# Kernel tuning notes

Measured on AMD Instinct MI355X. Metric: run time of the kernel, lower is better.

## Reference

```python
import jax, jax.numpy as jnp
import numpy as np

B = 8192      # batch of matchups
L = 40        # history_len
HN = 32       # hist_numeric_dim
TE = 96       # team_embed_dim
SE = 32       # seed_embed_dim
HH = 64       # hist_hidden_dim
NH = 4        # num_heads
HD = HH // NH # head dim = 16
MID = 128     # middle_dim
BOX = 8       # box_score_dim
NT = 400      # num_teams
NS = 17       # num_seeds
TOWER_IN = TE + SE + 1 + 2 * HH  # 257
MERGED = 2 * MID                 # 256
EPS = 1e-5


def setup_inputs() -> dict:
    key = jax.random.key(0)
    ks = iter(jax.random.split(key, 80))
    nrm = lambda shape, s=0.05: (jax.random.normal(next(ks), shape, jnp.float32) * s)
    inp = {}
    inp['teamA_id'] = jax.random.randint(next(ks), (B,), 1, NT)
    inp['teamB_id'] = jax.random.randint(next(ks), (B,), 1, NT)
    inp['teamA_seed'] = jax.random.randint(next(ks), (B,), 0, NS)
    inp['teamB_seed'] = jax.random.randint(next(ks), (B,), 0, NS)
    inp['teamA_elo'] = 1500.0 + 200.0 * jax.random.normal(next(ks), (B,), jnp.float32)
    inp['teamB_elo'] = 1500.0 + 200.0 * jax.random.normal(next(ks), (B,), jnp.float32)
    inp['teamA_hist_numeric'] = jax.random.normal(next(ks), (B, L, HN), jnp.float32)
    inp['teamB_hist_numeric'] = jax.random.normal(next(ks), (B, L, HN), jnp.float32)
    inp['teamA_hist_opp_ids'] = jax.random.randint(next(ks), (B, L), 0, NT)
    inp['teamB_hist_opp_ids'] = jax.random.randint(next(ks), (B, L), 0, NT)
    # 0/1 padding mask; guarantee at least one valid game per row
    inp['teamA_hist_mask'] = (jax.random.uniform(next(ks), (B, L)) < 0.8).astype(jnp.float32).at[:, 0].set(1.0)
    inp['teamB_hist_mask'] = (jax.random.uniform(next(ks), (B, L)) < 0.8).astype(jnp.float32).at[:, 0].set(1.0)
    # parameters
    inp['team_emb'] = nrm((NT, TE), 0.1).at[0].set(0.0)  # padding_idx=0
    inp['seed_emb'] = nrm((NS, SE), 0.1)
    inp['conv_w'] = nrm((HH, HN + TE, 3))
    inp['conv_b'] = nrm((HH,))
    inp['cbn_g'] = jnp.ones((HH,)); inp['cbn_b'] = jnp.zeros((HH,))
    inp['cbn_rm'] = nrm((HH,), 0.01); inp['cbn_rv'] = jnp.ones((HH,))
    inp['hp_w'] = nrm((HH, HN + TE)); inp['hp_b'] = nrm((HH,))
    inp['qp_w'] = nrm((HH, TE)); inp['qp_b'] = nrm((HH,))
    inp['attn_in_w'] = nrm((3 * HH, HH)); inp['attn_in_b'] = nrm((3 * HH,))
    inp['attn_out_w'] = nrm((HH, HH)); inp['attn_out_b'] = nrm((HH,))
    inp['ln_g'] = jnp.ones((HH,)); inp['ln_b'] = jnp.zeros((HH,))
    inp['tw_w'] = nrm((MID, TOWER_IN)); inp['tw_b'] = nrm((MID,))
    inp['tbn_g'] = jnp.ones((MID,)); inp['tbn_b'] = jnp.zeros((MID,))
    inp['tbn_rm'] = nrm((MID,), 0.01); inp['tbn_rv'] = jnp.ones((MID,))
    inp['r1_w'] = nrm((MERGED, MERGED)); inp['r1_b'] = nrm((MERGED,))
    inp['r1bn_g'] = jnp.ones((MERGED,)); inp['r1bn_b'] = jnp.zeros((MERGED,))
    inp['r1bn_rm'] = nrm((MERGED,), 0.01); inp['r1bn_rv'] = jnp.ones((MERGED,))
    inp['r2_w'] = nrm((MERGED, MERGED)); inp['r2_b'] = nrm((MERGED,))
    inp['r2bn_g'] = jnp.ones((MERGED,)); inp['r2bn_b'] = jnp.zeros((MERGED,))
    inp['r2bn_rm'] = nrm((MERGED,), 0.01); inp['r2bn_rv'] = jnp.ones((MERGED,))
    inp['mu_w'] = nrm((BOX, MERGED)); inp['mu_b'] = nrm((BOX,))
    inp['lv_w'] = nrm((BOX, MERGED)); inp['lv_b'] = nrm((BOX,))
    inp['wl_w'] = nrm((1, MERGED)); inp['wl_b'] = nrm((1,))
    return inp


def _bn(x, g, b, rm, rv):
    # eval-mode BatchNorm over last axis
    return (x - rm) * jax.lax.rsqrt(rv + EPS) * g + b


def _ln(x, g, b):
    m = jnp.mean(x, axis=-1, keepdims=True)
    v = jnp.var(x, axis=-1, keepdims=True)
    return (x - m) * jax.lax.rsqrt(v + EPS) * g + b


def reference(teamA_id, teamB_id, teamA_seed, teamB_seed, teamA_elo, teamB_elo,
              teamA_hist_numeric, teamA_hist_opp_ids, teamA_hist_mask,
              teamB_hist_numeric, teamB_hist_opp_ids, teamB_hist_mask,
              team_emb, seed_emb, conv_w, conv_b, cbn_g, cbn_b, cbn_rm, cbn_rv,
              hp_w, hp_b, qp_w, qp_b, attn_in_w, attn_in_b, attn_out_w, attn_out_b,
              ln_g, ln_b, tw_w, tw_b, tbn_g, tbn_b, tbn_rm, tbn_rv,
              r1_w, r1_b, r1bn_g, r1bn_b, r1bn_rm, r1bn_rv,
              r2_w, r2_b, r2bn_g, r2bn_b, r2bn_rm, r2bn_rv,
              mu_w, mu_b, lv_w, lv_b, wl_w, wl_b):
    silu = jax.nn.silu

    def attend(q_emb, hn, opp, mask):
        m = mask[..., None]
        x = jnp.concatenate([hn * m, team_emb[opp] * m], axis=-1)      # [B,L,HN+TE]
        res = silu(x @ hp_w.T + hp_b)                                   # [B,L,HH]
        c = jax.lax.conv_general_dilated(
            x.transpose(0, 2, 1), conv_w, (1,), [(1, 1)],
            dimension_numbers=('NCH', 'OIH', 'NCH')) + conv_b[:, None]  # [B,HH,L]
        c = _bn(c.transpose(0, 2, 1), cbn_g, cbn_b, cbn_rm, cbn_rv)     # [B,L,HH]
        kv = silu(c + res)                                              # [B,L,HH]
        q = q_emb @ qp_w.T + qp_b                                       # [B,HH]
        wq, wk, wv = jnp.split(attn_in_w, 3, axis=0)
        bq, bk, bv = jnp.split(attn_in_b, 3, axis=0)
        qh = (q @ wq.T + bq).reshape(-1, NH, HD)
        kh = (kv @ wk.T + bk).reshape(-1, L, NH, HD)
        vh = (kv @ wv.T + bv).reshape(-1, L, NH, HD)
        scores = jnp.einsum('bhd,blhd->bhl', qh, kh) / np.float32(np.sqrt(HD))
        scores = jnp.where(mask[:, None, :] > 0.0, scores, -1e9)
        a = jax.nn.softmax(scores, axis=-1)
        o = jnp.einsum('bhl,blhd->bhd', a, vh).reshape(-1, HH)
        o = o @ attn_out_w.T + attn_out_b
        return _ln(o + q, ln_g, ln_b)

    ea = team_emb[teamA_id]
    eb = team_emb[teamB_id]
    sa = seed_emb[teamA_seed]
    sb = seed_emb[teamB_seed]
    za = (teamA_elo[:, None] - 1500.0) / 400.0
    zb = (teamB_elo[:, None] - 1500.0) / 400.0

    aa = attend(ea, teamA_hist_numeric, teamA_hist_opp_ids, teamA_hist_mask)
    ab = attend(ea, teamB_hist_numeric, teamB_hist_opp_ids, teamB_hist_mask)
    bb = attend(eb, teamB_hist_numeric, teamB_hist_opp_ids, teamB_hist_mask)
    ba = attend(eb, teamA_hist_numeric, teamA_hist_opp_ids, teamA_hist_mask)

    ta = jnp.concatenate([ea, sa, za, aa, ab], axis=-1)
    tb = jnp.concatenate([eb, sb, zb, bb, ba], axis=-1)

    tower = lambda t: silu(_bn(t @ tw_w.T + tw_b, tbn_g, tbn_b, tbn_rm, tbn_rv))
    ra = tower(ta)
    rb = tower(tb)

    x = jnp.concatenate([ra - rb, ra * rb], axis=-1)
    x = silu(_bn(x @ r1_w.T + r1_b, r1bn_g, r1bn_b, r1bn_rm, r1bn_rv)) + x
    x = silu(_bn(x @ r2_w.T + r2_b, r2bn_g, r2bn_b, r2bn_rm, r2bn_rv)) + x

    box_mu = x @ mu_w.T + mu_b
    box_log_var = x @ lv_w.T + lv_b
    win_logit = (x @ wl_w.T + wl_b)[:, 0]
    return ((box_mu, box_log_var), win_logit)
```

## Files before the change

kernel.cpp:

```cpp
#include <hip/hip_runtime.h>
#include <stdint.h>

#define EPS 1e-5f

typedef __attribute__((ext_vector_type(8))) short short8;
typedef __attribute__((ext_vector_type(4))) float floatx4;
typedef __attribute__((ext_vector_type(4))) unsigned uintx4;
typedef unsigned short u16;

__device__ __forceinline__ u16 f2bf(float f) {
  unsigned u = __builtin_bit_cast(unsigned, f);
  u += 0x7fffu + ((u >> 16) & 1u);
  return (u16)(u >> 16);
}
__device__ __forceinline__ float bf2f(u16 h) {
  return __builtin_bit_cast(float, (unsigned)h << 16);
}
__device__ __forceinline__ unsigned pack2bf(float a, float b) {
  return (unsigned)f2bf(a) | ((unsigned)f2bf(b) << 16);
}
__device__ __forceinline__ float silu_f(float x) { return x / (1.f + __expf(-x)); }
__device__ __forceinline__ float wave_sum(float x) {
  for (int off = 32; off > 0; off >>= 1) x += __shfl_xor(x, off);
  return x;
}

__global__ void prep_kernel(const float* __restrict__ hp_w, const float* __restrict__ conv_w,
                            const float* __restrict__ attn_in_w,
                            const float* __restrict__ attn_out_w,
                            const float* __restrict__ tw_w, const float* __restrict__ r1_w,
                            const float* __restrict__ r2_w,
                            u16* __restrict__ w1f, u16* __restrict__ w2f,
                            float* __restrict__ woT,
                            float* __restrict__ twT, float* __restrict__ r1T,
                            float* __restrict__ r2T) {
  int t = blockIdx.x * 256 + threadIdx.x;
  if (t < 32768) {
    int j = t & 7, lane = (t >> 3) & 63, ks = (t >> 9) & 3, nt = (t >> 11) & 3, tp = t >> 13;
    int k = ks * 32 + ((lane >> 4) << 3) + j;
    int c = nt * 16 + (lane & 15);
    float v = (tp == 3) ? hp_w[c * 128 + k] : conv_w[c * 384 + k * 3 + tp];
    w1f[t] = f2bf(v);
  }
  if (t < 8192) {
    int j = t & 7, lane = (t >> 3) & 63, ks = (t >> 9) & 1, nt = t >> 10;
    int k = ks * 32 + ((lane >> 4) << 3) + j;
    int n = nt * 16 + (lane & 15);
    w2f[t] = f2bf(attn_in_w[(64 + n) * 64 + k]);
  }
  if (t < 1024) {
    int j = t & 63, k4 = t >> 6;
#pragma unroll
    for (int i = 0; i < 4; ++i)
      woT[(k4 * 64 + j) * 4 + i] = attn_out_w[j * 64 + k4 * 4 + i];
  }
  if (t < 8320) {
    int mid = t & 127, k4 = t >> 7;
#pragma unroll
    for (int i = 0; i < 4; ++i) {
      int k = k4 * 4 + i;
      twT[t * 4 + i] = (k < 257) ? tw_w[mid * 257 + k] : 0.f;
    }
  }
  if (t < 16384) {
    int o = t & 255, k4 = t >> 8;
#pragma unroll
    for (int i = 0; i < 4; ++i) {
      r1T[t * 4 + i] = r1_w[o * 256 + k4 * 4 + i];
      r2T[t * 4 + i] = r2_w[o * 256 + k4 * 4 + i];
    }
  }
}

__global__ __launch_bounds__(64) void team_kernel(
    const float* __restrict__ temb, const float* __restrict__ qp_w,
    const float* __restrict__ qp_b, const float* __restrict__ attn_in_w,
    const float* __restrict__ attn_in_b,
    float* __restrict__ Qg, float* __restrict__ QHg) {
  __shared__ float e[96];
  __shared__ float qv[64];
  const int t = blockIdx.x;
  const int o = threadIdx.x;
  for (int i = o; i < 96; i += 64) e[i] = temb[t * 96 + i];
  __syncthreads();
  float acc = qp_b[o];
  for (int k = 0; k < 96; ++k) acc += e[k] * qp_w[o * 96 + k];
  qv[o] = acc;
  Qg[t * 64 + o] = acc;
  __syncthreads();
  float acc2 = attn_in_b[o];
  for (int k = 0; k < 64; ++k) acc2 += qv[k] * attn_in_w[o * 64 + k];
  QHg[t * 64 + o] = acc2;
}

__global__ __launch_bounds__(256, 2) void attn_kernel(
    const int* __restrict__ idA, const int* __restrict__ idB,
    const float* __restrict__ hnA, const float* __restrict__ hnB,
    const int* __restrict__ oppA, const int* __restrict__ oppB,
    const float* __restrict__ mskA, const float* __restrict__ mskB,
    const float* __restrict__ temb, const float* __restrict__ conv_b,
    const float* __restrict__ cbn_g, const float* __restrict__ cbn_b,
    const float* __restrict__ cbn_rm, const float* __restrict__ cbn_rv,
    const float* __restrict__ hp_b,
    const float* __restrict__ attn_in_b, const float* __restrict__ attn_out_b,
    const float* __restrict__ ln_g, const float* __restrict__ ln_b,
    const u16* __restrict__ w1f, const u16* __restrict__ w2f,
    const float* __restrict__ woT,
    const float* __restrict__ Qg, const float* __restrict__ QHg,
    float* __restrict__ ATT) {
  __shared__ __align__(16) u16 arena[19488];
  u16* xs = arena;
  u16* kvb = arena + 5712;
  float* KVP = (float*)(arena + 9168);
  float* a_s = (float*)(arena + 5712);
  float* o_s = a_s + 8 * 40;
  float* qh_s = o_s + 2 * 64;

  const int tid = threadIdx.x;
  const int lane = tid & 63;
  const int wv = tid >> 6;
  const int qd = lane >> 4;
  const int l16 = lane & 15;

  const int c_lane = wv * 16 + l16;
  const float sc_c = rsqrtf(cbn_rv[c_lane] + EPS) * cbn_g[c_lane];
  const float sh_c = cbn_b[c_lane] - cbn_rm[c_lane] * sc_c;
  const float hpb_c = hp_b[c_lane];
  const float cvb_c = conv_b[c_lane];
  const float lng = ln_g[lane], lnb = ln_b[lane];
  const float aob = attn_out_b[lane];
  const float kb0 = attn_in_b[64 + (wv * 2 + 0) * 16 + l16];
  const float kb1 = attn_in_b[64 + (wv * 2 + 1) * 16 + l16];

  if (tid < 136) {
    xs[tid] = 0;
    xs[41 * 136 + tid] = 0;
  }
  __syncthreads();

  short8 w1r[4][4];
#pragma unroll
  for (int tp = 0; tp < 4; ++tp)
#pragma unroll
    for (int ks = 0; ks < 4; ++ks)
      w1r[tp][ks] = *reinterpret_cast<const short8*>(
          w1f + (((tp * 4 + wv) * 4 + ks) * 64 + lane) * 8);
  short8 w2r[2][2];
#pragma unroll
  for (int ntl = 0; ntl < 2; ++ntl)
#pragma unroll
    for (int ks = 0; ks < 2; ++ks)
      w2r[ntl][ks] = *reinterpret_cast<const short8*>(
          w2f + (((wv * 2 + ntl) * 2 + ks) * 64 + lane) * 8);

  unsigned xr[12];
  float mkr[3];
  {
    int np = blockIdx.x;
    int pb = np >> 1;
    const float* phn = (np & 1) ? hnB : hnA;
    const int* popp = (np & 1) ? oppB : oppA;
    const float* pmsk = (np & 1) ? mskB : mskA;
#pragma unroll
    for (int j = 0; j < 3; ++j) {
      int sidx = j * 256 + tid;
      int srow = sidx >> 4, scg = sidx & 15;
      if (srow < 40) {
        int mrow = pb * 40 + srow;
        mkr[j] = pmsk[mrow];
        const float* p = (scg < 4)
                             ? phn + (size_t)mrow * 32 + scg * 8
                             : temb + (size_t)popp[mrow] * 96 + (scg * 8 - 32);
        floatx4 f0 = *reinterpret_cast<const floatx4*>(p);
        floatx4 f1 = *reinterpret_cast<const floatx4*>(p + 4);
        xr[j * 4 + 0] = pack2bf(f0[0], f0[1]);
        xr[j * 4 + 1] = pack2bf(f0[2], f0[3]);
        xr[j * 4 + 2] = pack2bf(f1[0], f1[1]);
        xr[j * 4 + 3] = pack2bf(f1[2], f1[3]);
      } else {
        mkr[j] = 0.f;
        xr[j * 4 + 0] = xr[j * 4 + 1] = xr[j * 4 + 2] = xr[j * 4 + 3] = 0u;
      }
    }
  }

  float qreg = 0.f, qhreg = 0.f, m_l = 0.f;
  if (wv < 2) {
    int b0i = blockIdx.x >> 1, s0 = blockIdx.x & 1;
    int id0 = wv ? idB[b0i] : idA[b0i];
    qreg = Qg[id0 * 64 + lane];
    qhreg = QHg[id0 * 64 + lane];
    if (lane < 40) m_l = (s0 ? mskB : mskA)[b0i * 40 + lane];
  }

#pragma unroll 1
  for (int it = 0; it < 8; ++it) {
    int pair = blockIdx.x + it * 2048;
    int b = pair >> 1, s = pair & 1;

#pragma unroll
    for (int j = 0; j < 3; ++j) {
      int sidx = j * 256 + tid;
      int srow = sidx >> 4;
      if (srow < 40) {
        bool keep = mkr[j] != 0.f;
        uintx4 v;
        v[0] = keep ? xr[j * 4 + 0] : 0u;
        v[1] = keep ? xr[j * 4 + 1] : 0u;
        v[2] = keep ? xr[j * 4 + 2] : 0u;
        v[3] = keep ? xr[j * 4 + 3] : 0u;
        *reinterpret_cast<uintx4*>(xs + (srow + 1) * 136 + (sidx & 15) * 8) = v;
      }
    }
    __syncthreads();

    float pf[3][8];
    float mknew[3];
    {
      int np = (it < 7) ? pair + 2048 : pair;
      int pb = np >> 1;
      const float* phn = (np & 1) ? hnB : hnA;
      const int* popp = (np & 1) ? oppB : oppA;
      const float* pmsk = (np & 1) ? mskB : mskA;
#pragma unroll
      for (int j = 0; j < 3; ++j) {
        int sidx = j * 256 + tid;
        int srow = sidx >> 4, scg = sidx & 15;
        if (srow < 40) {
          int mrow = pb * 40 + srow;
          mknew[j] = pmsk[mrow];
          const float* p = (scg < 4)
                               ? phn + (size_t)mrow * 32 + scg * 8
                               : temb + (size_t)popp[mrow] * 96 + (scg * 8 - 32);
          *reinterpret_cast<floatx4*>(&pf[j][0]) = *reinterpret_cast<const floatx4*>(p);
          *reinterpret_cast<floatx4*>(&pf[j][4]) = *reinterpret_cast<const floatx4*>(p + 4);
        } else {
          mknew[j] = 0.f;
#pragma unroll
          for (int q = 0; q < 8; ++q) pf[j][q] = 0.f;
        }
      }
    }

#pragma unroll 1
    for (int mt = 0; mt < 3; ++mt) {
      floatx4 ach = {0.f, 0.f, 0.f, 0.f};
      floatx4 acv = {0.f, 0.f, 0.f, 0.f};
#pragma unroll
      for (int ks = 0; ks < 4; ++ks) {
        const u16* base = xs + (mt * 16 + l16) * 136 + ks * 32 + (qd << 3);
        short8 af0 = *reinterpret_cast<const short8*>(base);
        short8 af1 = *reinterpret_cast<const short8*>(base + 136);
        short8 af2 = *reinterpret_cast<const short8*>(base + 272);
        acv = __builtin_amdgcn_mfma_f32_16x16x32_bf16(af0, w1r[0][ks], acv, 0, 0, 0);
        acv = __builtin_amdgcn_mfma_f32_16x16x32_bf16(af1, w1r[1][ks], acv, 0, 0, 0);
        acv = __builtin_amdgcn_mfma_f32_16x16x32_bf16(af2, w1r[2][ks], acv, 0, 0, 0);
        ach = __builtin_amdgcn_mfma_f32_16x16x32_bf16(af1, w1r[3][ks], ach, 0, 0, 0);
      }
#pragma unroll
      for (int r = 0; r < 4; ++r) {
        float kv = silu_f(silu_f(ach[r] + hpb_c) + (acv[r] + cvb_c) * sc_c + sh_c);
        kvb[(mt * 16 + qd * 4 + r) * 72 + c_lane] = f2bf(kv);
      }
    }
    __syncthreads();

    {
      floatx4 acc[3][2] = {};
#pragma unroll
      for (int mt = 0; mt < 3; ++mt) {
        short8 af[2];
#pragma unroll
        for (int ks = 0; ks < 2; ++ks)
          af[ks] = *reinterpret_cast<const short8*>(
              kvb + (mt * 16 + l16) * 72 + ks * 32 + (qd << 3));
#pragma unroll
        for (int ntl = 0; ntl < 2; ++ntl)
#pragma unroll
          for (int ks = 0; ks < 2; ++ks)
            acc[mt][ntl] = __builtin_amdgcn_mfma_f32_16x16x32_bf16(
                af[ks], w2r[ntl][ks], acc[mt][ntl], 0, 0, 0);
      }
#pragma unroll
      for (int mt = 0; mt < 3; ++mt)
#pragma unroll
        for (int ntl = 0; ntl < 2; ++ntl)
#pragma unroll
          for (int r = 0; r < 4; ++r) {
            int row = mt * 16 + qd * 4 + r;
            if (row < 40)
              KVP[row * 129 + (wv * 2 + ntl) * 16 + l16] =
                  acc[mt][ntl][r] + (ntl ? kb1 : kb0);
          }
    }
    __syncthreads();

#pragma unroll
    for (int j = 0; j < 3; ++j) {
      xr[j * 4 + 0] = pack2bf(pf[j][0], pf[j][1]);
      xr[j * 4 + 1] = pack2bf(pf[j][2], pf[j][3]);
      xr[j * 4 + 2] = pack2bf(pf[j][4], pf[j][5]);
      xr[j * 4 + 3] = pack2bf(pf[j][6], pf[j][7]);
      mkr[j] = mknew[j];
    }

    if (wv < 2) {
      int qi = wv;
      qh_s[qi * 64 + lane] = qhreg;
      float a[4];
#pragma unroll
      for (int h = 0; h < 4; ++h) {
        float e = 0.f;
        if (lane < 40 && m_l > 0.f) {
          float s0 = 0.f, s1 = 0.f;
#pragma unroll
          for (int d = 0; d < 16; d += 2) {
            s0 += qh_s[qi * 64 + h * 16 + d] * KVP[lane * 129 + h * 16 + d];
            s1 += qh_s[qi * 64 + h * 16 + d + 1] * KVP[lane * 129 + h * 16 + d + 1];
          }
          e = __expf((s0 + s1) * 0.25f);
        }
        float sm = wave_sum(e);
        a[h] = e / sm;
      }
#pragma unroll
      for (int h = 0; h < 4; ++h)
        if (lane < 40) a_s[(qi * 4 + h) * 40 + lane] = a[h];
      {
        int p = qi * 4 + (lane >> 4);
        float v0 = 0.f, v1 = 0.f;
#pragma unroll
        for (int l = 0; l < 40; l += 2) {
          v0 += a_s[p * 40 + l] * KVP[l * 129 + 64 + lane];
          v1 += a_s[p * 40 + l + 1] * KVP[(l + 1) * 129 + 64 + lane];
        }
        o_s[qi * 64 + lane] = v0 + v1;
      }
      float acc0 = aob + qreg, acc1 = 0.f;
      const floatx4* wo4 = reinterpret_cast<const floatx4*>(woT);
#pragma unroll 8
      for (int k4 = 0; k4 < 16; ++k4) {
        floatx4 w4 = wo4[k4 * 64 + lane];
        floatx4 x4 = *reinterpret_cast<const floatx4*>(&o_s[qi * 64 + k4 * 4]);
        acc0 += x4[0] * w4[0] + x4[2] * w4[2];
        acc1 += x4[1] * w4[1] + x4[3] * w4[3];
      }
      float r = acc0 + acc1;
      float mean = wave_sum(r) * (1.f / 64.f);
      float dv = r - mean;
      float var = wave_sum(dv * dv) * (1.f / 64.f);
      float outv = dv * rsqrtf(var + EPS) * lng + lnb;
      ATT[((qi * 2 + s) * 8192 + b) * 64 + lane] = outv;

      if (it < 7) {
        int bn = b + 1024;
        int idn = wv ? idB[bn] : idA[bn];
        qreg = Qg[idn * 64 + lane];
        qhreg = QHg[idn * 64 + lane];
        m_l = (lane < 40) ? (s ? mskB : mskA)[bn * 40 + lane] : 0.f;
      }
    }
  }
}

__global__ __launch_bounds__(256) void head_kernel(
    const int* __restrict__ idA, const int* __restrict__ idB,
    const int* __restrict__ seedA, const int* __restrict__ seedB,
    const float* __restrict__ eloA, const float* __restrict__ eloB,
    const float* __restrict__ temb, const float* __restrict__ semb,
    const float* __restrict__ twT, const float* __restrict__ tw_b,
    const float* __restrict__ tbn_g, const float* __restrict__ tbn_b,
    const float* __restrict__ tbn_rm, const float* __restrict__ tbn_rv,
    const float* __restrict__ r1T, const float* __restrict__ r1_b,
    const float* __restrict__ r1bn_g, const float* __restrict__ r1bn_b,
    const float* __restrict__ r1bn_rm, const float* __restrict__ r1bn_rv,
    const float* __restrict__ r2T, const float* __restrict__ r2_b,
    const float* __restrict__ r2bn_g, const float* __restrict__ r2bn_b,
    const float* __restrict__ r2bn_rm, const float* __restrict__ r2bn_rv,
    const float* __restrict__ mu_w, const float* __restrict__ mu_b,
    const float* __restrict__ lv_w, const float* __restrict__ lv_b,
    const float* __restrict__ wl_w, const float* __restrict__ wl_b,
    const float* __restrict__ ATT, float* __restrict__ out) {
  __shared__ __align__(16) float smem[12416];
  float* tv = smem;
  float* rr = smem + 8320;
  float* xv = smem;
  float* xw = smem + 4096;
  const int tid = threadIdx.x;
  const int b0 = blockIdx.x * 16;

  for (int idx = tid; idx < 2 * 16 * 260; idx += 256) {
    int k = idx % 260;
    int bi = (idx / 260) & 15;
    int team = idx / (260 * 16);
    int b = b0 + bi;
    float v;
    if (k < 96) v = temb[(team ? idB[b] : idA[b]) * 96 + k];
    else if (k < 128) v = semb[(team ? seedB[b] : seedA[b]) * 32 + (k - 96)];
    else if (k == 128) v = ((team ? eloB[b] : eloA[b]) - 1500.f) * (1.f / 400.f);
    else if (k < 193) v = ATT[((team * 2 + team) * 8192 + b) * 64 + (k - 129)];
    else if (k < 257) v = ATT[((team * 2 + (1 - team)) * 8192 + b) * 64 + (k - 193)];
    else v = 0.f;
    tv[(team * 16 + bi) * 260 + k] = v;
  }
  __syncthreads();

  {
    int team = tid >> 7, mid = tid & 127;
    const floatx4* twv = reinterpret_cast<const floatx4*>(twT);
    float acc[16];
    float b_ = tw_b[mid];
#pragma unroll
    for (int bi = 0; bi < 16; ++bi) acc[bi] = b_;
#pragma unroll 2
    for (int k4 = 0; k4 < 65; ++k4) {
      floatx4 w4 = twv[k4 * 128 + mid];
#pragma unroll
      for (int bi = 0; bi < 16; ++bi) {
        floatx4 x4 = *reinterpret_cast<const floatx4*>(&tv[(team * 16 + bi) * 260 + k4 * 4]);
        acc[bi] += x4[0] * w4[0] + x4[1] * w4[1] + x4[2] * w4[2] + x4[3] * w4[3];
      }
    }
    float sc = rsqrtf(tbn_rv[mid] + EPS) * tbn_g[mid];
    float sh = tbn_b[mid] - tbn_rm[mid] * sc;
#pragma unroll
    for (int bi = 0; bi < 16; ++bi)
      rr[(team * 16 + bi) * 128 + mid] = silu_f(acc[bi] * sc + sh);
  }
  __syncthreads();
  {
    int o = tid;
#pragma unroll
    for (int bi = 0; bi < 16; ++bi)
      xv[bi * 256 + o] = (o < 128)
                             ? (rr[bi * 128 + o] - rr[(16 + bi) * 128 + o])
                             : (rr[bi * 128 + o - 128] * rr[(16 + bi) * 128 + o - 128]);
  }
  __syncthreads();
  {
    int o = tid;
    const floatx4* r1v = reinterpret_cast<const floatx4*>(r1T);
    float acc[16];
    float b_ = r1_b[o];
#pragma unroll
    for (int bi = 0; bi < 16; ++bi) acc[bi] = b_;
#pragma unroll 2
    for (int k4 = 0; k4 < 64; ++k4) {
      floatx4 w4 = r1v[k4 * 256 + o];
#pragma unroll
      for (int bi = 0; bi < 16; ++bi) {
        floatx4 x4 = *reinterpret_cast<const floatx4*>(&xv[bi * 256 + k4 * 4]);
        acc[bi] += x4[0] * w4[0] + x4[1] * w4[1] + x4[2] * w4[2] + x4[3] * w4[3];
      }
    }
    float sc = rsqrtf(r1bn_rv[o] + EPS) * r1bn_g[o];
    float sh = r1bn_b[o] - r1bn_rm[o] * sc;
#pragma unroll
    for (int bi = 0; bi < 16; ++bi)
      xw[bi * 256 + o] = silu_f(acc[bi] * sc + sh) + xv[bi * 256 + o];
  }
  __syncthreads();
  {
    int o = tid;
    const floatx4* r2v = reinterpret_cast<const floatx4*>(r2T);
    float acc[16];
    float b_ = r2_b[o];
#pragma unroll
    for (int bi = 0; bi < 16; ++bi) acc[bi] = b_;
#pragma unroll 2
    for (int k4 = 0; k4 < 64; ++k4) {
      floatx4 w4 = r2v[k4 * 256 + o];
#pragma unroll
      for (int bi = 0; bi < 16; ++bi) {
        floatx4 x4 = *reinterpret_cast<const floatx4*>(&xw[bi * 256 + k4 * 4]);
        acc[bi] += x4[0] * w4[0] + x4[1] * w4[1] + x4[2] * w4[2] + x4[3] * w4[3];
      }
    }
    float sc = rsqrtf(r2bn_rv[o] + EPS) * r2bn_g[o];
    float sh = r2bn_b[o] - r2bn_rm[o] * sc;
#pragma unroll
    for (int bi = 0; bi < 16; ++bi)
      xv[bi * 256 + o] = silu_f(acc[bi] * sc + sh) + xw[bi * 256 + o];
  }
  __syncthreads();
  {
    int bi = tid >> 4, j = tid & 15;
    const float* wrow = (j < 8) ? (mu_w + j * 256) : (lv_w + (j - 8) * 256);
    const floatx4* wrow4 = reinterpret_cast<const floatx4*>(wrow);
    float acc = (j < 8) ? mu_b[j] : lv_b[j - 8];
#pragma unroll 4
    for (int k4 = 0; k4 < 64; ++k4) {
      floatx4 x4 = *reinterpret_cast<const floatx4*>(&xv[bi * 256 + k4 * 4]);
      floatx4 w4 = wrow4[k4];
      acc += x4[0] * w4[0] + x4[1] * w4[1] + x4[2] * w4[2] + x4[3] * w4[3];
    }
    int b = b0 + bi;
    if (j < 8) out[b * 8 + j] = acc;
    else out[65536 + b * 8 + (j - 8)] = acc;
    if (tid < 16) {
      const floatx4* wl4 = reinterpret_cast<const floatx4*>(wl_w);
      float acc2 = wl_b[0];
#pragma unroll 4
      for (int k4 = 0; k4 < 64; ++k4) {
        floatx4 x4 = *reinterpret_cast<const floatx4*>(&xv[tid * 256 + k4 * 4]);
        floatx4 w4 = wl4[k4];
        acc2 += x4[0] * w4[0] + x4[1] * w4[1] + x4[2] * w4[2] + x4[3] * w4[3];
      }
      out[131072 + b0 + tid] = acc2;
    }
  }
}

extern "C" void kernel_launch(void* const* d_in, const int* in_sizes, int n_in,
                              void* d_out, int out_size, void* d_ws, size_t ws_size,
                              hipStream_t stream) {
  const int* idA = (const int*)d_in[0];
  const int* idB = (const int*)d_in[1];
  const int* seedA = (const int*)d_in[2];
  const int* seedB = (const int*)d_in[3];
  const float* eloA = (const float*)d_in[4];
  const float* eloB = (const float*)d_in[5];
  const float* hnA = (const float*)d_in[6];
  const float* hnB = (const float*)d_in[7];
  const int* oppA = (const int*)d_in[8];
  const int* oppB = (const int*)d_in[9];
  const float* mskA = (const float*)d_in[10];
  const float* mskB = (const float*)d_in[11];
  const float* temb = (const float*)d_in[12];
  const float* semb = (const float*)d_in[13];
  const float* conv_w = (const float*)d_in[14];
  const float* conv_b = (const float*)d_in[15];
  const float* cbn_g = (const float*)d_in[16];
  const float* cbn_b = (const float*)d_in[17];
  const float* cbn_rm = (const float*)d_in[18];
  const float* cbn_rv = (const float*)d_in[19];
  const float* hp_w = (const float*)d_in[20];
  const float* hp_b = (const float*)d_in[21];
  const float* qp_w = (const float*)d_in[22];
  const float* qp_b = (const float*)d_in[23];
  const float* attn_in_w = (const float*)d_in[24];
  const float* attn_in_b = (const float*)d_in[25];
  const float* attn_out_w = (const float*)d_in[26];
  const float* attn_out_b = (const float*)d_in[27];
  const float* ln_g = (const float*)d_in[28];
  const float* ln_b = (const float*)d_in[29];
  const float* tw_w = (const float*)d_in[30];
  const float* tw_b = (const float*)d_in[31];
  const float* tbn_g = (const float*)d_in[32];
  const float* tbn_b = (const float*)d_in[33];
  const float* tbn_rm = (const float*)d_in[34];
  const float* tbn_rv = (const float*)d_in[35];
  const float* r1_w = (const float*)d_in[36];
  const float* r1_b = (const float*)d_in[37];
  const float* r1bn_g = (const float*)d_in[38];
  const float* r1bn_b = (const float*)d_in[39];
  const float* r1bn_rm = (const float*)d_in[40];
  const float* r1bn_rv = (const float*)d_in[41];
  const float* r2_w = (const float*)d_in[42];
  const float* r2_b = (const float*)d_in[43];
  const float* r2bn_g = (const float*)d_in[44];
  const float* r2bn_b = (const float*)d_in[45];
  const float* r2bn_rm = (const float*)d_in[46];
  const float* r2bn_rv = (const float*)d_in[47];
  const float* mu_w = (const float*)d_in[48];
  const float* mu_b = (const float*)d_in[49];
  const float* lv_w = (const float*)d_in[50];
  const float* lv_b = (const float*)d_in[51];
  const float* wl_w = (const float*)d_in[52];
  const float* wl_b = (const float*)d_in[53];

  char* ws = (char*)d_ws;
  u16* w1f = (u16*)(ws + 0);
  u16* w2f = (u16*)(ws + 65536);
  float* woT = (float*)(ws + 81920);
  float* Qg = (float*)(ws + 98304);
  float* QHg = (float*)(ws + 200704);
  float* twT = (float*)(ws + 303104);
  float* r1T = (float*)(ws + 436224);
  float* r2T = (float*)(ws + 698368);
  float* ATT = (float*)(ws + 960512);

  prep_kernel<<<256, 256, 0, stream>>>(hp_w, conv_w, attn_in_w, attn_out_w,
                                       tw_w, r1_w, r2_w,
                                       w1f, w2f, woT, twT, r1T, r2T);
  team_kernel<<<400, 64, 0, stream>>>(temb, qp_w, qp_b, attn_in_w, attn_in_b, Qg, QHg);
  attn_kernel<<<2048, 256, 0, stream>>>(idA, idB, hnA, hnB, oppA, oppB, mskA, mskB,
                                        temb, conv_b, cbn_g, cbn_b, cbn_rm, cbn_rv,
                                        hp_b, attn_in_b, attn_out_b, ln_g, ln_b,
                                        w1f, w2f, woT, Qg, QHg, ATT);
  head_kernel<<<512, 256, 0, stream>>>(idA, idB, seedA, seedB, eloA, eloB, temb, semb,
                                       twT, tw_b, tbn_g, tbn_b, tbn_rm, tbn_rv,
                                       r1T, r1_b, r1bn_g, r1bn_b, r1bn_rm, r1bn_rv,
                                       r2T, r2_b, r2bn_g, r2bn_b, r2bn_rm, r2bn_rv,
                                       mu_w, mu_b, lv_w, lv_b, wl_w, wl_b,
                                       ATT, (float*)d_out);
}
```

Baseline: 558.4 us.

## Spread attention epilogue across all four waves instead of two

The per-row attention tail (scores, softmax, weighted sum of values, output projection) previously ran on only two of four waves while the others idled. Now each wave handles two heads of one query, half of the value positions, and half of the output-projection K range. Partial results are combined through shared memory, and the layer norm stays on two waves. This adds three block-wide barriers per iteration and extra LDS traffic in exchange for better wave utilisation.

```diff
diff --git a/kernel.cpp b/kernel.cpp
--- a/kernel.cpp
+++ b/kernel.cpp
@@ -109,18 +109,21 @@
     const float* __restrict__ Qg, const float* __restrict__ QHg,
     float* __restrict__ ATT) {
   __shared__ __align__(16) u16 arena[19488];
+  __shared__ __align__(16) float qh_s[2 * 64];
   u16* xs = arena;
   u16* kvb = arena + 5712;
   float* KVP = (float*)(arena + 9168);
   float* a_s = (float*)(arena + 5712);
-  float* o_s = a_s + 8 * 40;
-  float* qh_s = o_s + 2 * 64;
+  float* op = a_s + 8 * 40;
+  float* rp = op + 2 * 2 * 64;
 
   const int tid = threadIdx.x;
   const int lane = tid & 63;
   const int wv = tid >> 6;
   const int qd = lane >> 4;
   const int l16 = lane & 15;
+  const int qw = wv >> 1;
+  const int hw = wv & 1;
 
   const int c_lane = wv * 16 + l16;
   const float sc_c = rsqrtf(cbn_rv[c_lane] + EPS) * cbn_g[c_lane];
@@ -185,12 +188,14 @@
   }
 
   float qreg = 0.f, qhreg = 0.f, m_l = 0.f;
-  if (wv < 2) {
+  {
     int b0i = blockIdx.x >> 1, s0 = blockIdx.x & 1;
-    int id0 = wv ? idB[b0i] : idA[b0i];
-    qreg = Qg[id0 * 64 + lane];
-    qhreg = QHg[id0 * 64 + lane];
     if (lane < 40) m_l = (s0 ? mskB : mskA)[b0i * 40 + lane];
+    if (wv < 2) {
+      int id0 = wv ? idB[b0i] : idA[b0i];
+      qreg = Qg[id0 * 64 + lane];
+      qhreg = QHg[id0 * 64 + lane];
+    }
   }
 
 #pragma unroll 1
@@ -198,6 +203,7 @@
     int pair = blockIdx.x + it * 2048;
     int b = pair >> 1, s = pair & 1;
 
+    if (wv < 2) qh_s[wv * 64 + lane] = qhreg;
 #pragma unroll
     for (int j = 0; j < 3; ++j) {
       int sidx = j * 256 + tid;
@@ -304,60 +310,77 @@
       mkr[j] = mknew[j];
     }
 
-    if (wv < 2) {
-      int qi = wv;
-      qh_s[qi * 64 + lane] = qhreg;
-      float a[4];
-#pragma unroll
-      for (int h = 0; h < 4; ++h) {
+    {
+      float a2[2];
+#pragma unroll
+      for (int hh = 0; hh < 2; ++hh) {
+        int h = hw * 2 + hh;
         float e = 0.f;
         if (lane < 40 && m_l > 0.f) {
           float s0 = 0.f, s1 = 0.f;
 #pragma unroll
           for (int d = 0; d < 16; d += 2) {
-            s0 += qh_s[qi * 64 + h * 16 + d] * KVP[lane * 129 + h * 16 + d];
-            s1 += qh_s[qi * 64 + h * 16 + d + 1] * KVP[lane * 129 + h * 16 + d + 1];
+            s0 += qh_s[qw * 64 + h * 16 + d] * KVP[lane * 129 + h * 16 + d];
+            s1 += qh_s[qw * 64 + h * 16 + d + 1] * KVP[lane * 129 + h * 16 + d + 1];
           }
           e = __expf((s0 + s1) * 0.25f);
         }
         float sm = wave_sum(e);
-        a[h] = e / sm;
-      }
-#pragma unroll
-      for (int h = 0; h < 4; ++h)
-        if (lane < 40) a_s[(qi * 4 + h) * 40 + lane] = a[h];
-      {
-        int p = qi * 4 + (lane >> 4);
-        float v0 = 0.f, v1 = 0.f;
-#pragma unroll
-        for (int l = 0; l < 40; l += 2) {
-          v0 += a_s[p * 40 + l] * KVP[l * 129 + 64 + lane];
-          v1 += a_s[p * 40 + l + 1] * KVP[(l + 1) * 129 + 64 + lane];
-        }
-        o_s[qi * 64 + lane] = v0 + v1;
-      }
-      float acc0 = aob + qreg, acc1 = 0.f;
+        a2[hh] = e / sm;
+      }
+      if (lane < 40) {
+        a_s[(qw * 4 + hw * 2 + 0) * 40 + lane] = a2[0];
+        a_s[(qw * 4 + hw * 2 + 1) * 40 + lane] = a2[1];
+      }
+    }
+    __syncthreads();
+
+    {
+      int p = qw * 4 + (lane >> 4);
+      int l0 = hw * 20;
+      float v0 = 0.f, v1 = 0.f;
+#pragma unroll
+      for (int l = l0; l < l0 + 20; l += 2) {
+        v0 += a_s[p * 40 + l] * KVP[l * 129 + 64 + lane];
+        v1 += a_s[p * 40 + l + 1] * KVP[(l + 1) * 129 + 64 + lane];
+      }
+      op[(qw * 2 + hw) * 64 + lane] = v0 + v1;
+    }
+    __syncthreads();
+
+    {
+      float acc0 = 0.f, acc1 = 0.f;
       const floatx4* wo4 = reinterpret_cast<const floatx4*>(woT);
-#pragma unroll 8
-      for (int k4 = 0; k4 < 16; ++k4) {
+#pragma unroll
+      for (int k4 = hw * 8; k4 < hw * 8 + 8; ++k4) {
         floatx4 w4 = wo4[k4 * 64 + lane];
-        floatx4 x4 = *reinterpret_cast<const floatx4*>(&o_s[qi * 64 + k4 * 4]);
-        acc0 += x4[0] * w4[0] + x4[2] * w4[2];
-        acc1 += x4[1] * w4[1] + x4[3] * w4[3];
-      }
-      float r = acc0 + acc1;
+        floatx4 xa = *reinterpret_cast<const floatx4*>(&op[(qw * 2 + 0) * 64 + k4 * 4]);
+        floatx4 xb = *reinterpret_cast<const floatx4*>(&op[(qw * 2 + 1) * 64 + k4 * 4]);
+        acc0 += (xa[0] + xb[0]) * w4[0] + (xa[2] + xb[2]) * w4[2];
+        acc1 += (xa[1] + xb[1]) * w4[1] + (xa[3] + xb[3]) * w4[3];
+      }
+      rp[(qw * 2 + hw) * 64 + lane] = acc0 + acc1;
+    }
+    __syncthreads();
+
+    if (wv < 2) {
+      int qi = wv;
+      float r = rp[(qi * 2 + 0) * 64 + lane] + rp[(qi * 2 + 1) * 64 + lane] +
+                aob + qreg;
       float mean = wave_sum(r) * (1.f / 64.f);
       float dv = r - mean;
       float var = wave_sum(dv * dv) * (1.f / 64.f);
       float outv = dv * rsqrtf(var + EPS) * lng + lnb;
       ATT[((qi * 2 + s) * 8192 + b) * 64 + lane] = outv;
-
-      if (it < 7) {
-        int bn = b + 1024;
+    }
+
+    if (it < 7) {
+      int bn = b + 1024;
+      if (lane < 40) m_l = (s ? mskB : mskA)[bn * 40 + lane];
+      if (wv < 2) {
         int idn = wv ? idB[bn] : idA[bn];
         qreg = Qg[idn * 64 + lane];
         qhreg = QHg[idn * 64 + lane];
-        m_l = (lane < 40) ? (s ? mskB : mskA)[bn * 40 + lane] : 0.f;
       }
     }
   }
```

Result: faster. 531.1 us (-4.9%).

## Process two histories per iteration so all four waves run attention

Applied to the files above, without the earlier changes.

The attention kernel now handles two batch rows per loop iteration, with double-buffered shared staging and KV buffers, so all four waves run the softmax/output stage (one query per wave) instead of only two waves working while the others idle. Iterations halve from 8 to 4, prefetch covers two rows plus the next query data, and __syncthreads is replaced with an explicit lgkmcnt wait plus s_barrier. Shared memory roughly doubles and register pressure rises from the doubled prefetch arrays, which may reduce occupancy under the 2-blocks-per-CU launch bound.

```diff
diff --git a/kernel.cpp b/kernel.cpp
--- a/kernel.cpp
+++ b/kernel.cpp
@@ -24,6 +24,12 @@
   for (int off = 32; off > 0; off >>= 1) x += __shfl_xor(x, off);
   return x;
 }
+
+#define BARRIER()                                         \
+  do {                                                    \
+    asm volatile("s_waitcnt lgkmcnt(0)" ::: "memory");    \
+    __builtin_amdgcn_s_barrier();                         \
+  } while (0)
 
 __global__ void prep_kernel(const float* __restrict__ hp_w, const float* __restrict__ conv_w,
                             const float* __restrict__ attn_in_w,
@@ -108,19 +114,30 @@
     const float* __restrict__ woT,
     const float* __restrict__ Qg, const float* __restrict__ QHg,
     float* __restrict__ ATT) {
-  __shared__ __align__(16) u16 arena[19488];
-  u16* xs = arena;
-  u16* kvb = arena + 5712;
-  float* KVP = (float*)(arena + 9168);
-  float* a_s = (float*)(arena + 5712);
-  float* o_s = a_s + 8 * 40;
-  float* qh_s = o_s + 2 * 64;
+  __shared__ __align__(16) u16 arena[38976];
+  __shared__ __align__(16) float qh_s[4 * 64];
+  u16* xs0 = arena;
+  u16* xs1 = arena + 5712;
+  u16* kvb0 = arena + 11424;
+  u16* kvb1 = arena + 14880;
+  float* KVP = (float*)(arena + 18336);
+  float* a_s = (float*)(arena + 11424);
+  float* op = a_s + 640;
 
   const int tid = threadIdx.x;
   const int lane = tid & 63;
   const int wv = tid >> 6;
   const int qd = lane >> 4;
   const int l16 = lane & 15;
+  const int tw = wv >> 1;
+  const int qi = wv & 1;
+
+  const int s = blockIdx.x & 1;
+  const int bbase = blockIdx.x >> 1;
+  const float* phn = s ? hnB : hnA;
+  const int* popp = s ? oppB : oppA;
+  const float* pmsk = s ? mskB : mskA;
+  const int* pid = qi ? idB : idA;
 
   const int c_lane = wv * 16 + l16;
   const float sc_c = rsqrtf(cbn_rv[c_lane] + EPS) * cbn_g[c_lane];
@@ -133,10 +150,11 @@
   const float kb1 = attn_in_b[64 + (wv * 2 + 1) * 16 + l16];
 
   if (tid < 136) {
-    xs[tid] = 0;
-    xs[41 * 136 + tid] = 0;
-  }
-  __syncthreads();
+    xs0[tid] = 0;
+    xs0[41 * 136 + tid] = 0;
+    xs1[tid] = 0;
+    xs1[41 * 136 + tid] = 0;
+  }
 
   short8 w1r[4][4];
 #pragma unroll
@@ -153,119 +171,136 @@
       w2r[ntl][ks] = *reinterpret_cast<const short8*>(
           w2f + (((wv * 2 + ntl) * 2 + ks) * 64 + lane) * 8);
 
-  unsigned xr[12];
-  float mkr[3];
-  {
-    int np = blockIdx.x;
-    int pb = np >> 1;
-    const float* phn = (np & 1) ? hnB : hnA;
-    const int* popp = (np & 1) ? oppB : oppA;
-    const float* pmsk = (np & 1) ? mskB : mskA;
+  unsigned xr[2][12];
+  float mkr[2][3];
+#pragma unroll
+  for (int t = 0; t < 2; ++t) {
+    int pb = bbase + t * 1024;
 #pragma unroll
     for (int j = 0; j < 3; ++j) {
       int sidx = j * 256 + tid;
       int srow = sidx >> 4, scg = sidx & 15;
       if (srow < 40) {
         int mrow = pb * 40 + srow;
-        mkr[j] = pmsk[mrow];
+        mkr[t][j] = pmsk[mrow];
         const float* p = (scg < 4)
                              ? phn + (size_t)mrow * 32 + scg * 8
                              : temb + (size_t)popp[mrow] * 96 + (scg * 8 - 32);
         floatx4 f0 = *reinterpret_cast<const floatx4*>(p);
         floatx4 f1 = *reinterpret_cast<const floatx4*>(p + 4);
-        xr[j * 4 + 0] = pack2bf(f0[0], f0[1]);
-        xr[j * 4 + 1] = pack2bf(f0[2], f0[3]);
-        xr[j * 4 + 2] = pack2bf(f1[0], f1[1]);
-        xr[j * 4 + 3] = pack2bf(f1[2], f1[3]);
+        xr[t][j * 4 + 0] = pack2bf(f0[0], f0[1]);
+        xr[t][j * 4 + 1] = pack2bf(f0[2], f0[3]);
+        xr[t][j * 4 + 2] = pack2bf(f1[0], f1[1]);
+        xr[t][j * 4 + 3] = pack2bf(f1[2], f1[3]);
       } else {
-        mkr[j] = 0.f;
-        xr[j * 4 + 0] = xr[j * 4 + 1] = xr[j * 4 + 2] = xr[j * 4 + 3] = 0u;
-      }
-    }
-  }
-
-  float qreg = 0.f, qhreg = 0.f, m_l = 0.f;
-  if (wv < 2) {
-    int b0i = blockIdx.x >> 1, s0 = blockIdx.x & 1;
-    int id0 = wv ? idB[b0i] : idA[b0i];
+        mkr[t][j] = 0.f;
+        xr[t][j * 4 + 0] = xr[t][j * 4 + 1] = xr[t][j * 4 + 2] = xr[t][j * 4 + 3] = 0u;
+      }
+    }
+  }
+
+  float qreg, qhreg, m_l = 0.f;
+  {
+    int b0 = bbase + tw * 1024;
+    int id0 = pid[b0];
     qreg = Qg[id0 * 64 + lane];
     qhreg = QHg[id0 * 64 + lane];
-    if (lane < 40) m_l = (s0 ? mskB : mskA)[b0i * 40 + lane];
-  }
+    if (lane < 40) m_l = pmsk[b0 * 40 + lane];
+  }
+  BARRIER();
 
 #pragma unroll 1
-  for (int it = 0; it < 8; ++it) {
-    int pair = blockIdx.x + it * 2048;
-    int b = pair >> 1, s = pair & 1;
-
-#pragma unroll
-    for (int j = 0; j < 3; ++j) {
-      int sidx = j * 256 + tid;
-      int srow = sidx >> 4;
-      if (srow < 40) {
-        bool keep = mkr[j] != 0.f;
-        uintx4 v;
-        v[0] = keep ? xr[j * 4 + 0] : 0u;
-        v[1] = keep ? xr[j * 4 + 1] : 0u;
-        v[2] = keep ? xr[j * 4 + 2] : 0u;
-        v[3] = keep ? xr[j * 4 + 3] : 0u;
-        *reinterpret_cast<uintx4*>(xs + (srow + 1) * 136 + (sidx & 15) * 8) = v;
-      }
-    }
-    __syncthreads();
-
-    float pf[3][8];
-    float mknew[3];
-    {
-      int np = (it < 7) ? pair + 2048 : pair;
-      int pb = np >> 1;
-      const float* phn = (np & 1) ? hnB : hnA;
-      const int* popp = (np & 1) ? oppB : oppA;
-      const float* pmsk = (np & 1) ? mskB : mskA;
+  for (int it = 0; it < 4; ++it) {
+    int bt0 = bbase + (2 * it) * 1024;
+    int bt1 = bt0 + 1024;
+    int b_w = bbase + (2 * it + tw) * 1024;
+
+#pragma unroll
+    for (int t = 0; t < 2; ++t) {
+      u16* xsd = t ? xs1 : xs0;
 #pragma unroll
       for (int j = 0; j < 3; ++j) {
         int sidx = j * 256 + tid;
-        int srow = sidx >> 4, scg = sidx & 15;
+        int srow = sidx >> 4;
         if (srow < 40) {
-          int mrow = pb * 40 + srow;
-          mknew[j] = pmsk[mrow];
-          const float* p = (scg < 4)
-                               ? phn + (size_t)mrow * 32 + scg * 8
-                               : temb + (size_t)popp[mrow] * 96 + (scg * 8 - 32);
-          *reinterpret_cast<floatx4*>(&pf[j][0]) = *reinterpret_cast<const floatx4*>(p);
-          *reinterpret_cast<floatx4*>(&pf[j][4]) = *reinterpret_cast<const floatx4*>(p + 4);
-        } else {
-          mknew[j] = 0.f;
-#pragma unroll
-          for (int q = 0; q < 8; ++q) pf[j][q] = 0.f;
+          bool keep = mkr[t][j] != 0.f;
+          uintx4 v;
+          v[0] = keep ? xr[t][j * 4 + 0] : 0u;
+          v[1] = keep ? xr[t][j * 4 + 1] : 0u;
+          v[2] = keep ? xr[t][j * 4 + 2] : 0u;
+          v[3] = keep ? xr[t][j * 4 + 3] : 0u;
+          *reinterpret_cast<uintx4*>(xsd + (srow + 1) * 136 + (sidx & 15) * 8) = v;
         }
       }
     }
+    BARRIER();
+
+    float pf[2][3][8];
+    float mknew[2][3];
+    float qn, qhn, m_n = 0.f;
+    {
+      int adv = (it < 3) ? 2048 : 0;
+#pragma unroll
+      for (int t = 0; t < 2; ++t) {
+        int pb = (t ? bt1 : bt0) + adv;
+#pragma unroll
+        for (int j = 0; j < 3; ++j) {
+          int sidx = j * 256 + tid;
+          int srow = sidx >> 4, scg = sidx & 15;
+          if (srow < 40) {
+            int mrow = pb * 40 + srow;
+            mknew[t][j] = pmsk[mrow];
+            const float* p = (scg < 4)
+                                 ? phn + (size_t)mrow * 32 + scg * 8
+                                 : temb + (size_t)popp[mrow] * 96 + (scg * 8 - 32);
+            *reinterpret_cast<floatx4*>(&pf[t][j][0]) = *reinterpret_cast<const floatx4*>(p);
+            *reinterpret_cast<floatx4*>(&pf[t][j][4]) = *reinterpret_cast<const floatx4*>(p + 4);
+          } else {
+            mknew[t][j] = 0.f;
+#pragma unroll
+            for (int q = 0; q < 8; ++q) pf[t][j][q] = 0.f;
+          }
+        }
+      }
+      int bn = b_w + adv;
+      int idn = pid[bn];
+      qn = Qg[idn * 64 + lane];
+      qhn = QHg[idn * 64 + lane];
+      if (lane < 40) m_n = pmsk[bn * 40 + lane];
+    }
 
 #pragma unroll 1
-    for (int mt = 0; mt < 3; ++mt) {
-      floatx4 ach = {0.f, 0.f, 0.f, 0.f};
-      floatx4 acv = {0.f, 0.f, 0.f, 0.f};
-#pragma unroll
-      for (int ks = 0; ks < 4; ++ks) {
-        const u16* base = xs + (mt * 16 + l16) * 136 + ks * 32 + (qd << 3);
-        short8 af0 = *reinterpret_cast<const short8*>(base);
-        short8 af1 = *reinterpret_cast<const short8*>(base + 136);
-        short8 af2 = *reinterpret_cast<const short8*>(base + 272);
-        acv = __builtin_amdgcn_mfma_f32_16x16x32_bf16(af0, w1r[0][ks], acv, 0, 0, 0);
-        acv = __builtin_amdgcn_mfma_f32_16x16x32_bf16(af1, w1r[1][ks], acv, 0, 0, 0);
-        acv = __builtin_amdgcn_mfma_f32_16x16x32_bf16(af2, w1r[2][ks], acv, 0, 0, 0);
-        ach = __builtin_amdgcn_mfma_f32_16x16x32_bf16(af1, w1r[3][ks], ach, 0, 0, 0);
-      }
-#pragma unroll
-      for (int r = 0; r < 4; ++r) {
-        float kv = silu_f(silu_f(ach[r] + hpb_c) + (acv[r] + cvb_c) * sc_c + sh_c);
-        kvb[(mt * 16 + qd * 4 + r) * 72 + c_lane] = f2bf(kv);
-      }
-    }
-    __syncthreads();
-
-    {
+    for (int t = 0; t < 2; ++t) {
+      const u16* xsrc = t ? xs1 : xs0;
+      u16* kdst = t ? kvb1 : kvb0;
+#pragma unroll 1
+      for (int mt = 0; mt < 3; ++mt) {
+        floatx4 ach = {0.f, 0.f, 0.f, 0.f};
+        floatx4 acv = {0.f, 0.f, 0.f, 0.f};
+#pragma unroll
+        for (int ks = 0; ks < 4; ++ks) {
+          const u16* base = xsrc + (mt * 16 + l16) * 136 + ks * 32 + (qd << 3);
+          short8 af0 = *reinterpret_cast<const short8*>(base);
+          short8 af1 = *reinterpret_cast<const short8*>(base + 136);
+          short8 af2 = *reinterpret_cast<const short8*>(base + 272);
+          acv = __builtin_amdgcn_mfma_f32_16x16x32_bf16(af0, w1r[0][ks], acv, 0, 0, 0);
+          acv = __builtin_amdgcn_mfma_f32_16x16x32_bf16(af1, w1r[1][ks], acv, 0, 0, 0);
+          acv = __builtin_amdgcn_mfma_f32_16x16x32_bf16(af2, w1r[2][ks], acv, 0, 0, 0);
+          ach = __builtin_amdgcn_mfma_f32_16x16x32_bf16(af1, w1r[3][ks], ach, 0, 0, 0);
+        }
+#pragma unroll
+        for (int r = 0; r < 4; ++r) {
+          float kv = silu_f(silu_f(ach[r] + hpb_c) + (acv[r] + cvb_c) * sc_c + sh_c);
+          kdst[(mt * 16 + qd * 4 + r) * 72 + c_lane] = f2bf(kv);
+        }
+      }
+    }
+    BARRIER();
+
+#pragma unroll 1
+    for (int t = 0; t < 2; ++t) {
+      const u16* ksrc = t ? kvb1 : kvb0;
+      float* Kp = KVP + t * 40 * 129;
       floatx4 acc[3][2] = {};
 #pragma unroll
       for (int mt = 0; mt < 3; ++mt) {
@@ -273,7 +308,7 @@
 #pragma unroll
         for (int ks = 0; ks < 2; ++ks)
           af[ks] = *reinterpret_cast<const short8*>(
-              kvb + (mt * 16 + l16) * 72 + ks * 32 + (qd << 3));
+              ksrc + (mt * 16 + l16) * 72 + ks * 32 + (qd << 3));
 #pragma unroll
         for (int ntl = 0; ntl < 2; ++ntl)
 #pragma unroll
@@ -289,25 +324,16 @@
           for (int r = 0; r < 4; ++r) {
             int row = mt * 16 + qd * 4 + r;
             if (row < 40)
-              KVP[row * 129 + (wv * 2 + ntl) * 16 + l16] =
+              Kp[row * 129 + (wv * 2 + ntl) * 16 + l16] =
                   acc[mt][ntl][r] + (ntl ? kb1 : kb0);
           }
     }
-    __syncthreads();
-
-#pragma unroll
-    for (int j = 0; j < 3; ++j) {
-      xr[j * 4 + 0] = pack2bf(pf[j][0], pf[j][1]);
-      xr[j * 4 + 1] = pack2bf(pf[j][2], pf[j][3]);
-      xr[j * 4 + 2] = pack2bf(pf[j][4], pf[j][5]);
-      xr[j * 4 + 3] = pack2bf(pf[j][6], pf[j][7]);
-      mkr[j] = mknew[j];
-    }
-
-    if (wv < 2) {
-      int qi = wv;
-      qh_s[qi * 64 + lane] = qhreg;
-      float a[4];
+    BARRIER();
+
+    {
+      const float* Kp = KVP + tw * 40 * 129;
+      qh_s[wv * 64 + lane] = qhreg;
+      float a4[4];
 #pragma unroll
       for (int h = 0; h < 4; ++h) {
         float e = 0.f;
@@ -315,33 +341,33 @@
           float s0 = 0.f, s1 = 0.f;
 #pragma unroll
           for (int d = 0; d < 16; d += 2) {
-            s0 += qh_s[qi * 64 + h * 16 + d] * KVP[lane * 129 + h * 16 + d];
-            s1 += qh_s[qi * 64 + h * 16 + d + 1] * KVP[lane * 129 + h * 16 + d + 1];
+            s0 += qh_s[wv * 64 + h * 16 + d] * Kp[lane * 129 + h * 16 + d];
+            s1 += qh_s[wv * 64 + h * 16 + d + 1] * Kp[lane * 129 + h * 16 + d + 1];
           }
           e = __expf((s0 + s1) * 0.25f);
         }
         float sm = wave_sum(e);
-        a[h] = e / sm;
+        a4[h] = e / sm;
       }
 #pragma unroll
       for (int h = 0; h < 4; ++h)
-        if (lane < 40) a_s[(qi * 4 + h) * 40 + lane] = a[h];
+        if (lane < 40) a_s[(wv * 4 + h) * 40 + lane] = a4[h];
       {
-        int p = qi * 4 + (lane >> 4);
+        int arow = wv * 4 + (lane >> 4);
         float v0 = 0.f, v1 = 0.f;
 #pragma unroll
         for (int l = 0; l < 40; l += 2) {
-          v0 += a_s[p * 40 + l] * KVP[l * 129 + 64 + lane];
-          v1 += a_s[p * 40 + l + 1] * KVP[(l + 1) * 129 + 64 + lane];
+          v0 += a_s[arow * 40 + l] * Kp[l * 129 + 64 + lane];
+          v1 += a_s[arow * 40 + l + 1] * Kp[(l + 1) * 129 + 64 + lane];
         }
-        o_s[qi * 64 + lane] = v0 + v1;
+        op[wv * 64 + lane] = v0 + v1;
       }
       float acc0 = aob + qreg, acc1 = 0.f;
       const floatx4* wo4 = reinterpret_cast<const floatx4*>(woT);
 #pragma unroll 8
       for (int k4 = 0; k4 < 16; ++k4) {
         floatx4 w4 = wo4[k4 * 64 + lane];
-        floatx4 x4 = *reinterpret_cast<const floatx4*>(&o_s[qi * 64 + k4 * 4]);
+        floatx4 x4 = *reinterpret_cast<const floatx4*>(&op[wv * 64 + k4 * 4]);
         acc0 += x4[0] * w4[0] + x4[2] * w4[2];
         acc1 += x4[1] * w4[1] + x4[3] * w4[3];
       }
@@ -350,16 +376,22 @@
       float dv = r - mean;
       float var = wave_sum(dv * dv) * (1.f / 64.f);
       float outv = dv * rsqrtf(var + EPS) * lng + lnb;
-      ATT[((qi * 2 + s) * 8192 + b) * 64 + lane] = outv;
-
-      if (it < 7) {
-        int bn = b + 1024;
-        int idn = wv ? idB[bn] : idA[bn];
-        qreg = Qg[idn * 64 + lane];
-        qhreg = QHg[idn * 64 + lane];
-        m_l = (lane < 40) ? (s ? mskB : mskA)[bn * 40 + lane] : 0.f;
-      }
-    }
+      ATT[((qi * 2 + s) * 8192 + b_w) * 64 + lane] = outv;
+    }
+
+#pragma unroll
+    for (int t = 0; t < 2; ++t)
+#pragma unroll
+      for (int j = 0; j < 3; ++j) {
+        xr[t][j * 4 + 0] = pack2bf(pf[t][j][0], pf[t][j][1]);
+        xr[t][j * 4 + 1] = pack2bf(pf[t][j][2], pf[t][j][3]);
+        xr[t][j * 4 + 2] = pack2bf(pf[t][j][4], pf[t][j][5]);
+        xr[t][j * 4 + 3] = pack2bf(pf[t][j][6], pf[t][j][7]);
+        mkr[t][j] = mknew[t][j];
+      }
+    qreg = qn;
+    qhreg = qhn;
+    m_l = m_n;
   }
 }
 
```

Result: faster. 547.0 us (-2.0%).
